# Kernel tuning notes

Hardware: AMD Instinct MI355X
Metric: run time of the kernel (lower is better)

Reference implementation:

```python
import jax, jax.numpy as jnp
import numpy as np

B, L, EMBED = 8, 4096, 1024
HEADS, WIN, SHIFT = 16, 128, 64
HD = EMBED // HEADS
MLP_HIDDEN = 4 * EMBED
SCALE = HD ** -0.5
NW = L // WIN


def _layer_norm(x, w, b, eps=1e-5):
    m = x.mean(-1, keepdims=True)
    v = x.var(-1, keepdims=True)
    return (x - m) * jax.lax.rsqrt(v + eps) * w + b


def _compute_mask():
    # replicate SwinBlock1D._compute_mask: region ids over full L, then windowed
    sizes = [L - WIN, WIN - SHIFT, SHIFT]
    region = np.zeros(L, np.int32)
    pos = 0
    for i, s in enumerate(sizes):
        region[pos:pos + s] = i
        pos += s
    region = region.reshape(NW, WIN)
    diff = region[:, None, :] - region[:, :, None]  # (nW, W, W)
    return jnp.asarray(np.where(diff != 0, -100.0, 0.0).astype(np.float32))


_MASK = _compute_mask()
_REL_IDX = jnp.arange(WIN)[None, :] - jnp.arange(WIN)[:, None] + WIN - 1  # (W, W)


def setup_inputs() -> dict:
    key = jax.random.key(0)
    ks = jax.random.split(key, 8)
    s = 0.02

    def w(k, shape):
        return jax.random.normal(k, shape, jnp.float32) * s

    return {
        "x": jax.random.normal(ks[0], (B, L, EMBED), jnp.float32),
        "qkv_w": w(ks[1], (3 * EMBED, EMBED)),
        "qkv_b": jnp.zeros((3 * EMBED,), jnp.float32),
        "proj_w": w(ks[2], (EMBED, EMBED)),
        "proj_b": jnp.zeros((EMBED,), jnp.float32),
        "rpb": w(ks[3], (2 * WIN - 1, HEADS)),
        "norm1_w": jnp.ones((EMBED,), jnp.float32),
        "norm1_b": jnp.zeros((EMBED,), jnp.float32),
        "norm2_w": jnp.ones((EMBED,), jnp.float32),
        "norm2_b": jnp.zeros((EMBED,), jnp.float32),
        "mlp_w1": w(ks[4], (MLP_HIDDEN, EMBED)),
        "mlp_b1": jnp.zeros((MLP_HIDDEN,), jnp.float32),
        "mlp_w2": w(ks[5], (EMBED, MLP_HIDDEN)),
        "mlp_b2": jnp.zeros((EMBED,), jnp.float32),
    }


def reference(x, qkv_w, qkv_b, proj_w, proj_b, rpb,
              norm1_w, norm1_b, norm2_w, norm2_b,
              mlp_w1, mlp_b1, mlp_w2, mlp_b2):
    BW = B * NW
    shortcut = x
    h = _layer_norm(x, norm1_w, norm1_b)
    # shifted-window attention (shift_size > 0)
    h = jnp.roll(h, -SHIFT, axis=1)
    win = h.reshape(BW, WIN, EMBED)
    qkv = (win @ qkv_w.T + qkv_b).reshape(BW, WIN, 3, HEADS, HD)
    qkv = qkv.transpose(2, 0, 3, 1, 4)  # (3, BW, H, W, hd)
    q, k, v = qkv[0], qkv[1], qkv[2]
    attn = jnp.einsum('bhqd,bhkd->bhqk', q, k) * SCALE
    bias = rpb[_REL_IDX]  # (W, W, H)
    attn = attn + bias.transpose(2, 0, 1)[None]
    attn = attn.reshape(B, NW, HEADS, WIN, WIN) + _MASK[None, :, None]
    attn = jax.nn.softmax(attn.reshape(BW, HEADS, WIN, WIN), axis=-1)
    # dropout layers are identity in eval mode
    out = jnp.einsum('bhqk,bhkd->bhqd', attn, v)
    out = out.transpose(0, 2, 1, 3).reshape(BW, WIN, EMBED)
    out = out @ proj_w.T + proj_b
    out = out.reshape(B, L, EMBED)
    out = jnp.roll(out, SHIFT, axis=1)
    x = shortcut + out
    # MLP block
    h2 = _layer_norm(x, norm2_w, norm2_b)
    h2 = jax.nn.gelu(h2 @ mlp_w1.T + mlp_b1, approximate=False) @ mlp_w2.T + mlp_b2
    return x + h2
```

## Files before the change

kernel.cpp:

```cpp
#include <hip/hip_runtime.h>
#include <cstdint>
#include <cstddef>

#define SEQ_L   4096
#define EMBED   1024
#define HEADS   16
#define WINSZ   128
#define SHIFTSZ 64
#define HD      64
#define NWIN    32
#define MTOT    32768
#define ATT_SCALE 0.125f

typedef __bf16 bf16x8 __attribute__((ext_vector_type(8)));
typedef float  f32x4  __attribute__((ext_vector_type(4)));

typedef __attribute__((address_space(3))) void       lds_void;
typedef const __attribute__((address_space(1))) void gbl_void;

#define GLDS16(g, s) __builtin_amdgcn_global_load_lds((gbl_void*)(g), (lds_void*)(s), 16, 0, 0)

__device__ __forceinline__ unsigned short f2bf(float f) {
    unsigned int u = __float_as_uint(f);
    u += 0x7fffu + ((u >> 16) & 1u);
    return (unsigned short)(u >> 16);
}

__launch_bounds__(256)
__global__ void wconv(const float* __restrict__ in, unsigned short* __restrict__ out, int n)
{
    const int i = (blockIdx.x * 256 + threadIdx.x) * 4;
    if (i < n) {
        const float4 v = *(const float4*)(in + i);
        ushort4 o;
        o.x = f2bf(v.x); o.y = f2bf(v.y); o.z = f2bf(v.z); o.w = f2bf(v.w);
        *(ushort4*)(out + i) = o;
    }
}

__launch_bounds__(256)
__global__ void ln_kernel(const float* __restrict__ x, const float* __restrict__ gw,
                          const float* __restrict__ gb, unsigned short* __restrict__ out,
                          int shift)
{
    const int row = blockIdx.x;
    const int b   = row >> 12;
    const int lw  = row & 4095;
    const int src = (b << 12) | ((lw + shift) & 4095);
    const int t   = threadIdx.x;

    const float4 v = ((const float4*)(x + (size_t)src * EMBED))[t];
    float s = v.x + v.y + v.z + v.w;
    float q = v.x * v.x + v.y * v.y + v.z * v.z + v.w * v.w;
#pragma unroll
    for (int off = 32; off > 0; off >>= 1) {
        s += __shfl_down(s, off);
        q += __shfl_down(q, off);
    }
    __shared__ float ss[4], qq[4];
    if ((t & 63) == 0) { ss[t >> 6] = s; qq[t >> 6] = q; }
    __syncthreads();
    s = ss[0] + ss[1] + ss[2] + ss[3];
    q = qq[0] + qq[1] + qq[2] + qq[3];
    const float mean = s * (1.0f / 1024.0f);
    const float rstd = rsqrtf(q * (1.0f / 1024.0f) - mean * mean + 1e-5f);

    const float4 w4 = ((const float4*)gw)[t];
    const float4 b4 = ((const float4*)gb)[t];
    ushort4 o;
    o.x = f2bf((v.x - mean) * rstd * w4.x + b4.x);
    o.y = f2bf((v.y - mean) * rstd * w4.y + b4.y);
    o.z = f2bf((v.z - mean) * rstd * w4.z + b4.z);
    o.w = f2bf((v.w - mean) * rstd * w4.w + b4.w);
    ((ushort4*)(out + (size_t)row * EMBED))[t] = o;
}


__device__ __forceinline__ void stage_half(const unsigned short* __restrict__ g, int ldk,
                                           char* ldsbase, int tid)
{
    const int r  = tid >> 3;
    const int cg = ((tid & 7) ^ (r & 7)) << 3;
    GLDS16(g + (size_t)r        * ldk + cg, ldsbase + tid * 16);
    GLDS16(g + (size_t)(r + 64) * ldk + cg, ldsbase + 8192 + tid * 16);
}

__device__ __forceinline__ bf16x8 lds_frag(const char* half, int row, int koff)
{
    const int off = koff ^ ((row & 7) << 4);
    return *(const bf16x8*)(half + row * 128 + off);
}

template<int EPI>
__launch_bounds__(512, 2)
__global__ void gemm256(const unsigned short* __restrict__ A, const unsigned short* __restrict__ W,
                        const float* __restrict__ bias, void* __restrict__ outv,
                        const float* __restrict__ resid, int M, int N, int K)
{
    __shared__ __align__(16) char lds[131072];
    const int tid = threadIdx.x;
    const int l   = tid & 63, w = tid >> 6;
    const int wm  = w >> 2, wn = w & 3;
    const int lr  = l & 15, hi = l >> 4;
    const int k0off = hi << 4;

    int id = blockIdx.x;
    const int nwg = gridDim.x;
    id = (id & 7) * (nwg >> 3) + (id >> 3);
    const int Ntl = N >> 8;
    const int m0  = (id / Ntl) << 8;
    const int n0  = (id % Ntl) << 8;
    const int NT  = K >> 6;

#define HTB(b, ab, h) (lds + ((((b) << 1 | (ab)) << 1 | (h)) << 14))

    stage_half(A + (size_t)m0         * K,      K, HTB(0,0,0), tid);
    stage_half(A + (size_t)(m0 + 128) * K,      K, HTB(0,0,1), tid);
    stage_half(W + (size_t)n0         * K,      K, HTB(0,1,0), tid);
    stage_half(W + (size_t)(n0 + 128) * K,      K, HTB(0,1,1), tid);
    stage_half(W + (size_t)n0         * K + 64, K, HTB(1,1,0), tid);
    stage_half(W + (size_t)(n0 + 128) * K + 64, K, HTB(1,1,1), tid);
    asm volatile("s_waitcnt vmcnt(4)" ::: "memory");
    __builtin_amdgcn_s_barrier();

    f32x4 acc[8][4];
#pragma unroll
    for (int f = 0; f < 8; ++f)
#pragma unroll
        for (int n = 0; n < 4; ++n)
            acc[f][n] = (f32x4){0.f, 0.f, 0.f, 0.f};

    bf16x8 bf[4][2], af[2][2];

#define LOAD_A(F0)                                                         \
    af[0][0] = lds_frag(Ah, (F0) * 16 + lr,      k0off);                   \
    af[0][1] = lds_frag(Ah, (F0) * 16 + lr,      64 + k0off);              \
    af[1][0] = lds_frag(Ah, (F0) * 16 + 16 + lr, k0off);                   \
    af[1][1] = lds_frag(Ah, (F0) * 16 + 16 + lr, 64 + k0off);

#define MFMA_BLOCK(F0)                                                     \
    __builtin_amdgcn_s_barrier();                                          \
    asm volatile("s_waitcnt lgkmcnt(0)" ::: "memory");                     \
    __builtin_amdgcn_s_setprio(1);                                         \
    _Pragma("unroll")                                                      \
    for (int n = 0; n < 4; ++n) {                                          \
        acc[F0][n]     = __builtin_amdgcn_mfma_f32_16x16x32_bf16(af[0][0], bf[n][0], acc[F0][n], 0, 0, 0);     \
        acc[F0][n]     = __builtin_amdgcn_mfma_f32_16x16x32_bf16(af[0][1], bf[n][1], acc[F0][n], 0, 0, 0);     \
        acc[F0 + 1][n] = __builtin_amdgcn_mfma_f32_16x16x32_bf16(af[1][0], bf[n][0], acc[F0 + 1][n], 0, 0, 0); \
        acc[F0 + 1][n] = __builtin_amdgcn_mfma_f32_16x16x32_bf16(af[1][1], bf[n][1], acc[F0 + 1][n], 0, 0, 0); \
    }                                                                      \
    __builtin_amdgcn_s_setprio(0);

    for (int t = 0; t < NT; ++t) {
        const int b = t & 1;
        const char* Ah = HTB(b, 0, wm);
        const char* Bh = HTB(b, 1, wn >> 1);
        const int   br0 = (wn & 1) << 6;
        const unsigned short* An = A + (size_t)m0 * K + (t + 1) * 64;
        const unsigned short* Wn = W + (size_t)n0 * K + (t + 2) * 64;

#pragma unroll
        for (int n = 0; n < 4; ++n) {
            bf[n][0] = lds_frag(Bh, br0 + n * 16 + lr, k0off);
            bf[n][1] = lds_frag(Bh, br0 + n * 16 + lr, 64 + k0off);
        }
        LOAD_A(0)
        if (t + 1 < NT) stage_half(An, K, HTB(b ^ 1, 0, 0), tid);
        MFMA_BLOCK(0)
        __builtin_amdgcn_s_barrier();

        LOAD_A(2)
        if (t + 1 < NT) stage_half(An + (size_t)128 * K, K, HTB(b ^ 1, 0, 1), tid);
        MFMA_BLOCK(2)
        __builtin_amdgcn_s_barrier();

        LOAD_A(4)
        if (t + 2 < NT) stage_half(Wn, K, HTB(b, 1, 0), tid);
        MFMA_BLOCK(4)
        __builtin_amdgcn_s_barrier();

        LOAD_A(6)
        if (t + 2 < NT) stage_half(Wn + (size_t)128 * K, K, HTB(b, 1, 1), tid);
        MFMA_BLOCK(6)
        if (t + 2 < NT) { asm volatile("s_waitcnt vmcnt(4)" ::: "memory"); }
        else            { asm volatile("s_waitcnt vmcnt(0)" ::: "memory"); }
        __builtin_amdgcn_s_barrier();
    }
#undef LOAD_A
#undef MFMA_BLOCK
#undef HTB

    const int cb = n0 + wn * 64;
    float bv[4];
#pragma unroll
    for (int n = 0; n < 4; ++n) bv[n] = bias[cb + n * 16 + lr];

#pragma unroll
    for (int f = 0; f < 8; ++f) {
        const int mbase = m0 + wm * 128 + f * 16 + hi * 4;
#pragma unroll
        for (int n = 0; n < 4; ++n) {
            const int col = cb + n * 16 + lr;
#pragma unroll
            for (int r = 0; r < 4; ++r) {
                const int m = mbase + r;
                float v = acc[f][n][r] + bv[n];
                if constexpr (EPI == 0) {
                    ((unsigned short*)outv)[(size_t)m * N + col] = f2bf(v);
                } else if constexpr (EPI == 1) {
                    const int bb = m >> 12;
                    const int lw = m & 4095;
                    const int ll = (lw + SHIFTSZ) & 4095;
                    const size_t di = ((size_t)(bb << 12) + ll) * (size_t)N + col;
                    ((float*)outv)[di] = resid[di] + v;
                } else if constexpr (EPI == 2) {
                    const float g = 0.5f * v * (1.0f + erff(v * 0.70710678118654752f));
                    ((unsigned short*)outv)[(size_t)m * N + col] = f2bf(g);
                } else {
                    float* o = (float*)outv;
                    const size_t di = (size_t)m * N + col;
                    o[di] = o[di] + v;
                }
            }
        }
    }
}

__launch_bounds__(256, 2)
__global__ void attn_kernel(const unsigned short* __restrict__ qkv, const float* __restrict__ rpb,
                            unsigned short* __restrict__ outp)
{
    __shared__ __align__(16) unsigned short P[WINSZ][136];
    __shared__ __align__(16) unsigned short VT[HD][136];

    const int t   = threadIdx.x;
    const int l   = t & 63;
    const int w   = t >> 6;
    const int lr  = l & 15;
    const int lq  = l >> 4;
    const int lk  = lq * 8;
    const int blk = blockIdx.x;
    const int win = blk >> 4;
    const int h   = blk & 15;
    const bool masked = ((win & (NWIN - 1)) == NWIN - 1);

    const unsigned short* qb = qkv + (size_t)(win * WINSZ) * (3 * EMBED) + h * HD;
    const unsigned short* kb = qb + EMBED;
    const unsigned short* vb = qb + 2 * EMBED;

    for (int idx = t; idx < WINSZ * HD; idx += 256) {
        const int k = idx >> 6;
        const int d = idx & 63;
        VT[d][k] = vb[(size_t)k * (3 * EMBED) + d];
    }

    const int mrow = w * 32;
    f32x4 sacc[2][8];
#pragma unroll
    for (int a = 0; a < 2; ++a)
#pragma unroll
        for (int b = 0; b < 8; ++b)
            sacc[a][b] = (f32x4){0.f, 0.f, 0.f, 0.f};

#pragma unroll
    for (int ks = 0; ks < 2; ++ks) {
        const int k0 = ks * 32;
        bf16x8 aq[2], bk8[8];
#pragma unroll
        for (int mi = 0; mi < 2; ++mi)
            aq[mi] = *(const bf16x8*)(qb + (size_t)(mrow + mi * 16 + lr) * (3 * EMBED) + k0 + lk);
#pragma unroll
        for (int ni = 0; ni < 8; ++ni)
            bk8[ni] = *(const bf16x8*)(kb + (size_t)(ni * 16 + lr) * (3 * EMBED) + k0 + lk);
#pragma unroll
        for (int mi = 0; mi < 2; ++mi)
#pragma unroll
            for (int ni = 0; ni < 8; ++ni)
                sacc[mi][ni] = __builtin_amdgcn_mfma_f32_16x16x32_bf16(aq[mi], bk8[ni], sacc[mi][ni], 0, 0, 0);
    }

#pragma unroll
    for (int mi = 0; mi < 2; ++mi)
#pragma unroll
        for (int r = 0; r < 4; ++r) {
            const int i = mrow + mi * 16 + lq * 4 + r;
            float v[8];
            float mx = -1e30f;
#pragma unroll
            for (int ni = 0; ni < 8; ++ni) {
                const int j = ni * 16 + lr;
                float sv = sacc[mi][ni][r] * ATT_SCALE + rpb[(j - i + WINSZ - 1) * HEADS + h];
                if (masked && ((i >= SHIFTSZ) != (j >= SHIFTSZ))) sv -= 100.0f;
                v[ni] = sv;
                mx = fmaxf(mx, sv);
            }
#pragma unroll
            for (int s = 1; s < 16; s <<= 1) mx = fmaxf(mx, __shfl_xor(mx, s));
            float sm = 0.f;
#pragma unroll
            for (int ni = 0; ni < 8; ++ni) {
                const float p = __expf(v[ni] - mx);
                v[ni] = p;
                sm += p;
            }
#pragma unroll
            for (int s = 1; s < 16; s <<= 1) sm += __shfl_xor(sm, s);
            const float rs = 1.0f / sm;
#pragma unroll
            for (int ni = 0; ni < 8; ++ni)
                P[i][ni * 16 + lr] = f2bf(v[ni] * rs);
        }

    __syncthreads();

    f32x4 oacc[2][4];
#pragma unroll
    for (int a = 0; a < 2; ++a)
#pragma unroll
        for (int b = 0; b < 4; ++b)
            oacc[a][b] = (f32x4){0.f, 0.f, 0.f, 0.f};

#pragma unroll
    for (int ks = 0; ks < 4; ++ks) {
        const int k0 = ks * 32;
        bf16x8 ap[2], av[4];
#pragma unroll
        for (int mi = 0; mi < 2; ++mi)
            ap[mi] = *(const bf16x8*)(&P[mrow + mi * 16 + lr][k0 + lk]);
#pragma unroll
        for (int ni = 0; ni < 4; ++ni)
            av[ni] = *(const bf16x8*)(&VT[ni * 16 + lr][k0 + lk]);
#pragma unroll
        for (int mi = 0; mi < 2; ++mi)
#pragma unroll
            for (int ni = 0; ni < 4; ++ni)
                oacc[mi][ni] = __builtin_amdgcn_mfma_f32_16x16x32_bf16(ap[mi], av[ni], oacc[mi][ni], 0, 0, 0);
    }

    unsigned short* ob = outp + (size_t)(win * WINSZ) * EMBED + h * HD;
#pragma unroll
    for (int mi = 0; mi < 2; ++mi)
#pragma unroll
        for (int ni = 0; ni < 4; ++ni)
#pragma unroll
            for (int r = 0; r < 4; ++r) {
                const int i = mrow + mi * 16 + lq * 4 + r;
                const int d = ni * 16 + lr;
                ob[(size_t)i * EMBED + d] = f2bf(oacc[mi][ni][r]);
            }
}

extern "C" void kernel_launch(void* const* d_in, const int* in_sizes, int n_in,
                              void* d_out, int out_size, void* d_ws, size_t ws_size,
                              hipStream_t stream)
{
    const float* x      = (const float*)d_in[0];
    const float* qkv_w  = (const float*)d_in[1];
    const float* qkv_b  = (const float*)d_in[2];
    const float* proj_w = (const float*)d_in[3];
    const float* proj_b = (const float*)d_in[4];
    const float* rpb    = (const float*)d_in[5];
    const float* n1w    = (const float*)d_in[6];
    const float* n1b    = (const float*)d_in[7];
    const float* n2w    = (const float*)d_in[8];
    const float* n2b    = (const float*)d_in[9];
    const float* w1     = (const float*)d_in[10];
    const float* b1     = (const float*)d_in[11];
    const float* w2     = (const float*)d_in[12];
    const float* b2     = (const float*)d_in[13];
    float* out = (float*)d_out;

    unsigned short* wqkv  = (unsigned short*)d_ws;
    unsigned short* wproj = wqkv  + (size_t)3072 * 1024;
    unsigned short* wm1   = wproj + (size_t)1024 * 1024;
    unsigned short* wm2   = wm1   + (size_t)4096 * 1024;
    unsigned short* bufA  = wm2   + (size_t)4096 * 1024;
    unsigned short* bufB  = bufA  + (size_t)MTOT * EMBED;

    wconv<<<3072, 256, 0, stream>>>(qkv_w, wqkv, 3 * EMBED * EMBED);
    wconv<<<1024, 256, 0, stream>>>(proj_w, wproj, EMBED * EMBED);
    wconv<<<4096, 256, 0, stream>>>(w1, wm1, 4 * EMBED * EMBED);
    wconv<<<4096, 256, 0, stream>>>(w2, wm2, 4 * EMBED * EMBED);

    ln_kernel<<<MTOT, 256, 0, stream>>>(x, n1w, n1b, bufA, SHIFTSZ);

    gemm256<0><<<dim3(1536), 512, 0, stream>>>(bufA, wqkv, qkv_b, bufB, nullptr, MTOT, 3 * EMBED, EMBED);

    attn_kernel<<<4096, 256, 0, stream>>>(bufB, rpb, bufA);

    gemm256<1><<<dim3(512), 512, 0, stream>>>(bufA, wproj, proj_b, out, x, MTOT, EMBED, EMBED);

    ln_kernel<<<MTOT, 256, 0, stream>>>(out, n2w, n2b, bufA, 0);

    for (int c = 0; c < 2; ++c) {
        const size_t r0 = (size_t)c * 16384;
        gemm256<2><<<dim3(1024), 512, 0, stream>>>(bufA + r0 * EMBED, wm1, b1, bufB, nullptr,
                                                   16384, 4 * EMBED, EMBED);
        gemm256<3><<<dim3(256), 512, 0, stream>>>(bufB, wm2, b2, out + r0 * EMBED, nullptr,
                                                  16384, EMBED, 4 * EMBED);
    }
}
```

Baseline: 1.276 ms.

## Double-buffer GEMM A fragments, stage attention K/V in LDS, warp-per-row LayerNorm

The GEMM main loop now alternates two register banks of A fragments and prefetches the next tile's A and B fragments during the last MFMA block. Finer lgkmcnt waits replace the full waits, and the loop is unrolled by two to fix the buffer index. The attention kernel stages K through async global-to-LDS loads with an XOR swizzle and builds a swizzled V-transpose from vector loads instead of scalar global reads. LayerNorm handles one row per wavefront with xor shuffles, dropping the shared-memory reduction and block barrier. These raise register and LDS pressure, and the unroll assumes NT is even.

```diff
diff --git a/kernel.cpp b/kernel.cpp
--- a/kernel.cpp
+++ b/kernel.cpp
@@ -43,36 +43,41 @@
                           const float* __restrict__ gb, unsigned short* __restrict__ out,
                           int shift)
 {
-    const int row = blockIdx.x;
-    const int b   = row >> 12;
-    const int lw  = row & 4095;
-    const int src = (b << 12) | ((lw + shift) & 4095);
-    const int t   = threadIdx.x;
-
-    const float4 v = ((const float4*)(x + (size_t)src * EMBED))[t];
-    float s = v.x + v.y + v.z + v.w;
-    float q = v.x * v.x + v.y * v.y + v.z * v.z + v.w * v.w;
+    const int row  = blockIdx.x * 4 + (threadIdx.x >> 6);
+    const int lane = threadIdx.x & 63;
+    const int b    = row >> 12;
+    const int lw   = row & 4095;
+    const int src  = (b << 12) | ((lw + shift) & 4095);
+    const float* xr = x + (size_t)src * EMBED;
+
+    float4 v[4];
+    float s = 0.f, q = 0.f;
+#pragma unroll
+    for (int j = 0; j < 4; ++j) {
+        v[j] = ((const float4*)xr)[lane + j * 64];
+        s += v[j].x + v[j].y + v[j].z + v[j].w;
+        q += v[j].x * v[j].x + v[j].y * v[j].y + v[j].z * v[j].z + v[j].w * v[j].w;
+    }
 #pragma unroll
     for (int off = 32; off > 0; off >>= 1) {
-        s += __shfl_down(s, off);
-        q += __shfl_down(q, off);
-    }
-    __shared__ float ss[4], qq[4];
-    if ((t & 63) == 0) { ss[t >> 6] = s; qq[t >> 6] = q; }
-    __syncthreads();
-    s = ss[0] + ss[1] + ss[2] + ss[3];
-    q = qq[0] + qq[1] + qq[2] + qq[3];
+        s += __shfl_xor(s, off);
+        q += __shfl_xor(q, off);
+    }
     const float mean = s * (1.0f / 1024.0f);
     const float rstd = rsqrtf(q * (1.0f / 1024.0f) - mean * mean + 1e-5f);
 
-    const float4 w4 = ((const float4*)gw)[t];
-    const float4 b4 = ((const float4*)gb)[t];
-    ushort4 o;
-    o.x = f2bf((v.x - mean) * rstd * w4.x + b4.x);
-    o.y = f2bf((v.y - mean) * rstd * w4.y + b4.y);
-    o.z = f2bf((v.z - mean) * rstd * w4.z + b4.z);
-    o.w = f2bf((v.w - mean) * rstd * w4.w + b4.w);
-    ((ushort4*)(out + (size_t)row * EMBED))[t] = o;
+    unsigned short* orow = out + (size_t)row * EMBED;
+#pragma unroll
+    for (int j = 0; j < 4; ++j) {
+        const float4 w4 = ((const float4*)gw)[lane + j * 64];
+        const float4 b4 = ((const float4*)gb)[lane + j * 64];
+        ushort4 o;
+        o.x = f2bf((v[j].x - mean) * rstd * w4.x + b4.x);
+        o.y = f2bf((v[j].y - mean) * rstd * w4.y + b4.y);
+        o.z = f2bf((v[j].z - mean) * rstd * w4.z + b4.z);
+        o.w = f2bf((v[j].w - mean) * rstd * w4.w + b4.w);
+        ((ushort4*)orow)[lane + j * 64] = o;
+    }
 }
 
 
@@ -103,6 +108,7 @@
     const int wm  = w >> 2, wn = w & 3;
     const int lr  = l & 15, hi = l >> 4;
     const int k0off = hi << 4;
+    const int br0   = (wn & 1) << 6;
 
     int id = blockIdx.x;
     const int nwg = gridDim.x;
@@ -130,64 +136,86 @@
         for (int n = 0; n < 4; ++n)
             acc[f][n] = (f32x4){0.f, 0.f, 0.f, 0.f};
 
-    bf16x8 bf[4][2], af[2][2];
-
-#define LOAD_A(F0)                                                         \
-    af[0][0] = lds_frag(Ah, (F0) * 16 + lr,      k0off);                   \
-    af[0][1] = lds_frag(Ah, (F0) * 16 + lr,      64 + k0off);              \
-    af[1][0] = lds_frag(Ah, (F0) * 16 + 16 + lr, k0off);                   \
-    af[1][1] = lds_frag(Ah, (F0) * 16 + 16 + lr, 64 + k0off);
-
-#define MFMA_BLOCK(F0)                                                     \
-    __builtin_amdgcn_s_barrier();                                          \
-    asm volatile("s_waitcnt lgkmcnt(0)" ::: "memory");                     \
-    __builtin_amdgcn_s_setprio(1);                                         \
-    _Pragma("unroll")                                                      \
-    for (int n = 0; n < 4; ++n) {                                          \
-        acc[F0][n]     = __builtin_amdgcn_mfma_f32_16x16x32_bf16(af[0][0], bf[n][0], acc[F0][n], 0, 0, 0);     \
-        acc[F0][n]     = __builtin_amdgcn_mfma_f32_16x16x32_bf16(af[0][1], bf[n][1], acc[F0][n], 0, 0, 0);     \
-        acc[F0 + 1][n] = __builtin_amdgcn_mfma_f32_16x16x32_bf16(af[1][0], bf[n][0], acc[F0 + 1][n], 0, 0, 0); \
-        acc[F0 + 1][n] = __builtin_amdgcn_mfma_f32_16x16x32_bf16(af[1][1], bf[n][1], acc[F0 + 1][n], 0, 0, 0); \
-    }                                                                      \
+    bf16x8 bf[4][2], af0[2][2], af1[2][2];
+
+#define LOAD_A_BANK(bank, AHP, F0)                                          \
+    af##bank[0][0] = lds_frag(AHP, (F0) * 16 + lr,      k0off);             \
+    af##bank[0][1] = lds_frag(AHP, (F0) * 16 + lr,      64 + k0off);        \
+    af##bank[1][0] = lds_frag(AHP, (F0) * 16 + 16 + lr, k0off);             \
+    af##bank[1][1] = lds_frag(AHP, (F0) * 16 + 16 + lr, 64 + k0off);
+
+#define MFMA_BANK(bank, F0)                                                 \
+    __builtin_amdgcn_s_setprio(1);                                          \
+    _Pragma("unroll")                                                       \
+    for (int n = 0; n < 4; ++n) {                                           \
+        acc[F0][n]     = __builtin_amdgcn_mfma_f32_16x16x32_bf16(af##bank[0][0], bf[n][0], acc[F0][n], 0, 0, 0);         \
+        acc[F0][n]     = __builtin_amdgcn_mfma_f32_16x16x32_bf16(af##bank[0][1], bf[n][1], acc[F0][n], 0, 0, 0);         \
+        acc[(F0) + 1][n] = __builtin_amdgcn_mfma_f32_16x16x32_bf16(af##bank[1][0], bf[n][0], acc[(F0) + 1][n], 0, 0, 0); \
+        acc[(F0) + 1][n] = __builtin_amdgcn_mfma_f32_16x16x32_bf16(af##bank[1][1], bf[n][1], acc[(F0) + 1][n], 0, 0, 0); \
+    }                                                                       \
     __builtin_amdgcn_s_setprio(0);
 
-    for (int t = 0; t < NT; ++t) {
-        const int b = t & 1;
-        const char* Ah = HTB(b, 0, wm);
-        const char* Bh = HTB(b, 1, wn >> 1);
-        const int   br0 = (wn & 1) << 6;
-        const unsigned short* An = A + (size_t)m0 * K + (t + 1) * 64;
-        const unsigned short* Wn = W + (size_t)n0 * K + (t + 2) * 64;
-
+    {
+        const char* Bh0 = HTB(0, 1, wn >> 1);
 #pragma unroll
         for (int n = 0; n < 4; ++n) {
-            bf[n][0] = lds_frag(Bh, br0 + n * 16 + lr, k0off);
-            bf[n][1] = lds_frag(Bh, br0 + n * 16 + lr, 64 + k0off);
+            bf[n][0] = lds_frag(Bh0, br0 + n * 16 + lr, k0off);
+            bf[n][1] = lds_frag(Bh0, br0 + n * 16 + lr, 64 + k0off);
         }
-        LOAD_A(0)
-        if (t + 1 < NT) stage_half(An, K, HTB(b ^ 1, 0, 0), tid);
-        MFMA_BLOCK(0)
-        __builtin_amdgcn_s_barrier();
-
-        LOAD_A(2)
-        if (t + 1 < NT) stage_half(An + (size_t)128 * K, K, HTB(b ^ 1, 0, 1), tid);
-        MFMA_BLOCK(2)
-        __builtin_amdgcn_s_barrier();
-
-        LOAD_A(4)
-        if (t + 2 < NT) stage_half(Wn, K, HTB(b, 1, 0), tid);
-        MFMA_BLOCK(4)
-        __builtin_amdgcn_s_barrier();
-
-        LOAD_A(6)
-        if (t + 2 < NT) stage_half(Wn + (size_t)128 * K, K, HTB(b, 1, 1), tid);
-        MFMA_BLOCK(6)
-        if (t + 2 < NT) { asm volatile("s_waitcnt vmcnt(4)" ::: "memory"); }
-        else            { asm volatile("s_waitcnt vmcnt(0)" ::: "memory"); }
-        __builtin_amdgcn_s_barrier();
-    }
-#undef LOAD_A
-#undef MFMA_BLOCK
+        const char* Ah0 = HTB(0, 0, wm);
+        LOAD_A_BANK(0, Ah0, 0)
+    }
+
+#define TILE(BUF)                                                              \
+    {                                                                          \
+        const char* Ah = HTB(BUF, 0, wm);                                      \
+        const unsigned short* An = A + (size_t)m0 * K + (size_t)(t + 1) * 64;  \
+        const unsigned short* Wn = W + (size_t)n0 * K + (size_t)(t + 2) * 64;  \
+                                                        \
+        LOAD_A_BANK(1, Ah, 2)                                                  \
+        if (t + 1 < NT) stage_half(An, K, HTB(BUF ^ 1, 0, 0), tid);            \
+        asm volatile("s_waitcnt lgkmcnt(4)" ::: "memory");                     \
+        MFMA_BANK(0, 0)                                                        \
+        __builtin_amdgcn_s_barrier();                                          \
+                                                        \
+        LOAD_A_BANK(0, Ah, 4)                                                  \
+        if (t + 1 < NT) stage_half(An + (size_t)128 * K, K, HTB(BUF ^ 1, 0, 1), tid); \
+        asm volatile("s_waitcnt lgkmcnt(4)" ::: "memory");                     \
+        MFMA_BANK(1, 2)                                                        \
+        __builtin_amdgcn_s_barrier();                                          \
+                                                        \
+        LOAD_A_BANK(1, Ah, 6)                                                  \
+        if (t + 2 < NT) stage_half(Wn, K, HTB(BUF, 1, 0), tid);                \
+        asm volatile("s_waitcnt lgkmcnt(4)" ::: "memory");                     \
+        MFMA_BANK(0, 4)                                                        \
+        __builtin_amdgcn_s_barrier();                                          \
+                                                        \
+        if (t + 2 < NT) { asm volatile("s_waitcnt vmcnt(2)" ::: "memory"); }   \
+        else            { asm volatile("s_waitcnt vmcnt(0)" ::: "memory"); }   \
+        if (t + 1 < NT) { const char* AhN = HTB(BUF ^ 1, 0, wm); LOAD_A_BANK(0, AhN, 0) } \
+        if (t + 2 < NT) stage_half(Wn + (size_t)128 * K, K, HTB(BUF, 1, 1), tid); \
+        if (t + 1 < NT) { asm volatile("s_waitcnt lgkmcnt(4)" ::: "memory"); } \
+        else            { asm volatile("s_waitcnt lgkmcnt(0)" ::: "memory"); } \
+        MFMA_BANK(1, 6)                                                        \
+        if (t + 1 < NT) {                                                      \
+            const char* BhN = HTB(BUF ^ 1, 1, wn >> 1);                        \
+            _Pragma("unroll")                                                  \
+            for (int n = 0; n < 4; ++n) {                                      \
+                bf[n][0] = lds_frag(BhN, br0 + n * 16 + lr, k0off);            \
+                bf[n][1] = lds_frag(BhN, br0 + n * 16 + lr, 64 + k0off);       \
+            }                                                                  \
+        }                                                                      \
+        __builtin_amdgcn_s_barrier();                                          \
+    }
+
+    int t;
+    for (int u = 0; u < (NT >> 1); ++u) {
+        t = 2 * u;     TILE(0)
+        t = 2 * u + 1; TILE(1)
+    }
+#undef TILE
+#undef LOAD_A_BANK
+#undef MFMA_BANK
 #undef HTB
 
     const int cb = n0 + wn * 64;
@@ -226,12 +254,19 @@
     }
 }
 
+__device__ __forceinline__ bf16x8 vt_frag(const char* vt, int d, int kbyte)
+{
+    const int key = ((d >> 3) & 7) << 4;
+    return *(const bf16x8*)(vt + d * 272 + (kbyte ^ key));
+}
+
 __launch_bounds__(256, 2)
 __global__ void attn_kernel(const unsigned short* __restrict__ qkv, const float* __restrict__ rpb,
                             unsigned short* __restrict__ outp)
 {
+    __shared__ __align__(16) char          Ks[128 * 128];
     __shared__ __align__(16) unsigned short P[WINSZ][136];
-    __shared__ __align__(16) unsigned short VT[HD][136];
+    __shared__ __align__(16) unsigned short VTl[64 * 136];
 
     const int t   = threadIdx.x;
     const int l   = t & 63;
@@ -248,11 +283,34 @@
     const unsigned short* kb = qb + EMBED;
     const unsigned short* vb = qb + 2 * EMBED;
 
-    for (int idx = t; idx < WINSZ * HD; idx += 256) {
-        const int k = idx >> 6;
-        const int d = idx & 63;
-        VT[d][k] = vb[(size_t)k * (3 * EMBED) + d];
-    }
+    {
+        const int c = t & 7;
+#pragma unroll
+        for (int p = 0; p < 4; ++p) {
+            const int r  = (t >> 3) + p * 32;
+            const int cg = (c ^ (r & 7)) << 3;
+            GLDS16(kb + (size_t)r * (3 * EMBED) + cg, Ks + p * 4096 + t * 16);
+        }
+    }
+    {
+        const int c = t & 7;
+#pragma unroll
+        for (int p = 0; p < 4; ++p) {
+            const int k = (t >> 3) + p * 32;
+            const uint4 v = *(const uint4*)(vb + (size_t)k * (3 * EMBED) + c * 8);
+            const unsigned int vals[4] = {v.x, v.y, v.z, v.w};
+            char* base = (char*)VTl;
+#pragma unroll
+            for (int e2 = 0; e2 < 4; ++e2) {
+                const int d0 = c * 8 + e2 * 2;
+                const int key = c << 4;
+                *(unsigned short*)(base + d0 * 272 + ((2 * k) ^ key))       = (unsigned short)(vals[e2] & 0xffff);
+                *(unsigned short*)(base + (d0 + 1) * 272 + ((2 * k) ^ key)) = (unsigned short)(vals[e2] >> 16);
+            }
+        }
+    }
+    asm volatile("s_waitcnt vmcnt(0)" ::: "memory");
+    __syncthreads();
 
     const int mrow = w * 32;
     f32x4 sacc[2][8];
@@ -264,14 +322,14 @@
 
 #pragma unroll
     for (int ks = 0; ks < 2; ++ks) {
-        const int k0 = ks * 32;
+        const int kby = ks * 64 + lq * 16;
         bf16x8 aq[2], bk8[8];
 #pragma unroll
         for (int mi = 0; mi < 2; ++mi)
-            aq[mi] = *(const bf16x8*)(qb + (size_t)(mrow + mi * 16 + lr) * (3 * EMBED) + k0 + lk);
+            aq[mi] = *(const bf16x8*)(qb + (size_t)(mrow + mi * 16 + lr) * (3 * EMBED) + ks * 32 + lk);
 #pragma unroll
         for (int ni = 0; ni < 8; ++ni)
-            bk8[ni] = *(const bf16x8*)(kb + (size_t)(ni * 16 + lr) * (3 * EMBED) + k0 + lk);
+            bk8[ni] = lds_frag(Ks, ni * 16 + lr, kby);
 #pragma unroll
         for (int mi = 0; mi < 2; ++mi)
 #pragma unroll
@@ -329,7 +387,7 @@
             ap[mi] = *(const bf16x8*)(&P[mrow + mi * 16 + lr][k0 + lk]);
 #pragma unroll
         for (int ni = 0; ni < 4; ++ni)
-            av[ni] = *(const bf16x8*)(&VT[ni * 16 + lr][k0 + lk]);
+            av[ni] = vt_frag((const char*)VTl, ni * 16 + lr, k0 * 2 + lq * 16);
 #pragma unroll
         for (int mi = 0; mi < 2; ++mi)
 #pragma unroll
@@ -382,7 +440,7 @@
     wconv<<<4096, 256, 0, stream>>>(w1, wm1, 4 * EMBED * EMBED);
     wconv<<<4096, 256, 0, stream>>>(w2, wm2, 4 * EMBED * EMBED);
 
-    ln_kernel<<<MTOT, 256, 0, stream>>>(x, n1w, n1b, bufA, SHIFTSZ);
+    ln_kernel<<<8192, 256, 0, stream>>>(x, n1w, n1b, bufA, SHIFTSZ);
 
     gemm256<0><<<dim3(1536), 512, 0, stream>>>(bufA, wqkv, qkv_b, bufB, nullptr, MTOT, 3 * EMBED, EMBED);
 
@@ -390,7 +448,7 @@
 
     gemm256<1><<<dim3(512), 512, 0, stream>>>(bufA, wproj, proj_b, out, x, MTOT, EMBED, EMBED);
 
-    ln_kernel<<<MTOT, 256, 0, stream>>>(out, n2w, n2b, bufA, 0);
+    ln_kernel<<<8192, 256, 0, stream>>>(out, n2w, n2b, bufA, 0);
 
     for (int c = 0; c < 2; ++c) {
         const size_t r0 = (size_t)c * 16384;
```

Result: faster. 1.230 ms (-3.6%).
